# Kernel optimization log

Hardware: AMD Instinct MI355X
Metric: run time of the kernel (lower is better)

The kernel has to match this reference:

```python
import jax, jax.numpy as jnp
import numpy as np

BLOCK = 16.0  # BLOCK_X == BLOCK_Y == 16


def setup_inputs() -> dict:
    key = jax.random.key(0)
    k1, k2, k3 = jax.random.split(key, 3)
    N = 4_000_000
    means3D = jax.random.normal(k1, (N, 3), dtype=jnp.float32)
    scales = jax.random.uniform(k2, (N, 3), dtype=jnp.float32, minval=0.005, maxval=0.05)
    rotations = jax.random.normal(k3, (N, 4), dtype=jnp.float32)  # unnormalized quats (r,x,y,z)
    # row-vector convention: p' = [x,y,z,1] @ M  (matches matrix[0]*x + matrix[4]*y + ... indexing)
    tanfovx, tanfovy = 0.8, 0.45
    znear, zfar = 0.01, 100.0
    view = np.eye(4, dtype=np.float32)
    view[3, 2] = 8.0  # camera translation: all points end up in front of camera
    proj_cam = np.zeros((4, 4), dtype=np.float32)
    proj_cam[0, 0] = 1.0 / tanfovx
    proj_cam[1, 1] = 1.0 / tanfovy
    proj_cam[2, 2] = zfar / (zfar - znear)
    proj_cam[2, 3] = 1.0
    proj_cam[3, 2] = -zfar * znear / (zfar - znear)
    projmatrix = view @ proj_cam  # full (view*proj), as in 3DGS
    return {
        "means3D": means3D,
        "scales": scales,
        "rotations": rotations,
        "viewmatrix": jnp.asarray(view),
        "projmatrix": jnp.asarray(projmatrix),
        "tanfovx": tanfovx,
        "tanfovy": tanfovy,
        "scale_modifier": 1.0,
        "image_height": 1080,
        "image_width": 1920,
    }


def reference(means3D, scales, rotations, viewmatrix, projmatrix,
              tanfovx, tanfovy, scale_modifier, image_height, image_width):
    H = float(image_height)
    W = float(image_width)
    focal_x = W / (2.0 * tanfovx)
    focal_y = H / (2.0 * tanfovy)

    # ---- projection (transformPoint4x3 / 4x4, row-vector convention) ----
    p_view = means3D @ viewmatrix[:3, :3] + viewmatrix[3, :3]        # [N,3]
    p_hom = means3D @ projmatrix[:3, :] + projmatrix[3, :]           # [N,4]
    p_w = 1.0 / (p_hom[:, 3] + 1e-7)
    p_proj = p_hom[:, :3] * p_w[:, None]

    # ---- computeCov3D: Sigma = (S R)^T (S R) ----
    r, x, y, z = rotations[:, 0], rotations[:, 1], rotations[:, 2], rotations[:, 3]
    R = jnp.stack([
        jnp.stack([1.0 - 2.0 * (y * y + z * z), 2.0 * (x * y - r * z), 2.0 * (x * z + r * y)], axis=-1),
        jnp.stack([2.0 * (x * y + r * z), 1.0 - 2.0 * (x * x + z * z), 2.0 * (y * z - r * x)], axis=-1),
        jnp.stack([2.0 * (x * z - r * y), 2.0 * (y * z + r * x), 1.0 - 2.0 * (x * x + y * y)], axis=-1),
    ], axis=-2)                                                      # [N,3,3]
    M = (scale_modifier * scales)[:, :, None] * R                    # S @ R: scale rows
    Sigma = jnp.einsum('nki,nkj->nij', M, M)                         # M^T M, symmetric [N,3,3]

    # ---- computeCov2D: EWA splatting Jacobian ----
    tz = p_view[:, 2]
    limx = 1.3 * tanfovx
    limy = 1.3 * tanfovy
    tx = jnp.clip(p_view[:, 0] / tz, -limx, limx) * tz
    ty = jnp.clip(p_view[:, 1] / tz, -limy, limy) * tz
    zeros = jnp.zeros_like(tz)
    # only the first two columns of J matter for the 2x2 cov
    col0 = jnp.stack([focal_x / tz, zeros, -(focal_x * tx) / (tz * tz)], axis=-1)  # [N,3]
    col1 = jnp.stack([zeros, focal_y / tz, -(focal_y * ty) / (tz * tz)], axis=-1)
    Jc = jnp.stack([col0, col1], axis=-1)                            # [N,3,2]
    W3 = viewmatrix[:3, :3]                                          # 3x3 rotation block
    T2 = jnp.einsum('ij,njk->nik', W3, Jc)                           # [N,3,2]
    cov2 = jnp.einsum('nki,nkl,nlj->nij', T2, Sigma, T2)             # [N,2,2]
    cov_x = cov2[:, 0, 0] + 0.3
    cov_y = cov2[:, 0, 1]
    cov_z = cov2[:, 1, 1] + 0.3

    # ---- screen-space radius from eigenvalues ----
    det = cov_x * cov_z - cov_y * cov_y
    mid = 0.5 * (cov_x + cov_z)
    lambda1 = mid + jnp.sqrt(jnp.maximum(0.1, mid * mid - det))      # lambda1 >= lambda2 always
    radius = jnp.ceil(3.0 * jnp.sqrt(lambda1))

    # ---- tile rect test (getRect) ----
    px = ((p_proj[:, 0] + 1.0) * W - 1.0) * 0.5                      # ndc2Pix
    py = ((p_proj[:, 1] + 1.0) * H - 1.0) * 0.5
    gx = (W + BLOCK - 1.0) / BLOCK
    gy = (H + BLOCK - 1.0) / BLOCK
    rmin_x = jnp.clip(jnp.floor((px - radius) / BLOCK), 0.0, gx)
    rmin_y = jnp.clip(jnp.floor((py - radius) / BLOCK), 0.0, gy)
    rmax_x = jnp.clip(jnp.floor((px + radius + BLOCK - 1.0) / BLOCK), 0.0, gx)
    rmax_y = jnp.clip(jnp.floor((py + radius + BLOCK - 1.0) / BLOCK), 0.0, gy)
    area = (rmax_x - rmin_x) * (rmax_y - rmin_y)

    # ---- culling (in_frustum + degenerate checks) ----
    valid = (tz > 0.2) & (det != 0.0) & (area != 0.0)
    radii = jnp.where(valid, radius, 0.0)
    return radii
```

## Files before the change

### kernel.cpp

```cpp
#include <hip/hip_runtime.h>


typedef float v4f __attribute__((ext_vector_type(4)));

__device__ __forceinline__ float frcp(float x)  { return __builtin_amdgcn_rcpf(x); }
__device__ __forceinline__ float fsqrt_(float x){ return __builtin_amdgcn_sqrtf(x); }

__device__ __forceinline__ v4f vrcp(v4f a) {
    v4f r; r.x = frcp(a.x); r.y = frcp(a.y); r.z = frcp(a.z); r.w = frcp(a.w); return r;
}
__device__ __forceinline__ v4f vsqrt(v4f a) {
    v4f r; r.x = fsqrt_(a.x); r.y = fsqrt_(a.y); r.z = fsqrt_(a.z); r.w = fsqrt_(a.w); return r;
}
__device__ __forceinline__ v4f vmaxs(v4f a, float b) {
    v4f r; r.x = fmaxf(a.x,b); r.y = fmaxf(a.y,b); r.z = fmaxf(a.z,b); r.w = fmaxf(a.w,b); return r;
}
__device__ __forceinline__ v4f vclamp(v4f a, float lo, float hi) {
    v4f r;
    r.x = fminf(fmaxf(a.x, lo), hi);
    r.y = fminf(fmaxf(a.y, lo), hi);
    r.z = fminf(fmaxf(a.z, lo), hi);
    r.w = fminf(fmaxf(a.w, lo), hi);
    return r;
}
__device__ __forceinline__ v4f vceil(v4f a) {
    v4f r; r.x = ceilf(a.x); r.y = ceilf(a.y); r.z = ceilf(a.z); r.w = ceilf(a.w); return r;
}

struct GaussChunk {
    v4f mx, my, mz;
    v4f qr, qx, qy, qz;
    v4f s0, s1, s2;
};

__device__ __forceinline__ v4f gauss_radii(
    const GaussChunk& c,
    const float* __restrict__ vmr, const float* __restrict__ pmr,
    float focal_x, float focal_y, float limx, float limy,
    float W, float H, float TX, float TY)
{
    const v4f pvx = c.mx*vmr[0] + c.my*vmr[4] + c.mz*vmr[8]  + vmr[12];
    const v4f pvy = c.mx*vmr[1] + c.my*vmr[5] + c.mz*vmr[9]  + vmr[13];
    const v4f tz  = c.mx*vmr[2] + c.my*vmr[6] + c.mz*vmr[10] + vmr[14];

    const v4f hx = c.mx*pmr[0] + c.my*pmr[4] + c.mz*pmr[8]  + pmr[12];
    const v4f hy = c.mx*pmr[1] + c.my*pmr[5] + c.mz*pmr[9]  + pmr[13];
    const v4f hw = c.mx*pmr[3] + c.my*pmr[7] + c.mz*pmr[11] + pmr[15];
    const v4f pw  = vrcp(hw + 1e-7f);
    const v4f ppx = hx * pw;
    const v4f ppy = hy * pw;

    const v4f itz = vrcp(tz);
    const v4f cx  = vclamp(pvx * itz, -limx, limx);
    const v4f cy  = vclamp(pvy * itz, -limy, limy);
    const v4f fxz = focal_x * itz;
    const v4f fyz = focal_y * itz;

    const v4f A0 = vmr[0] - vmr[2]*cx;
    const v4f A1 = vmr[4] - vmr[6]*cx;
    const v4f A2 = vmr[8] - vmr[10]*cx;
    const v4f B0 = vmr[1] - vmr[2]*cy;
    const v4f B1 = vmr[5] - vmr[6]*cy;
    const v4f B2 = vmr[9] - vmr[10]*cy;

    const v4f xx = c.qx*c.qx, yy = c.qy*c.qy, zz = c.qz*c.qz;
    const v4f xy = c.qx*c.qy, xz = c.qx*c.qz, yz = c.qy*c.qz;
    const v4f rx = c.qr*c.qx, ry = c.qr*c.qy, rz = c.qr*c.qz;
    const v4f R00 = 1.0f - 2.0f*(yy + zz);
    const v4f R01 = 2.0f*(xy - rz);
    const v4f R02 = 2.0f*(xz + ry);
    const v4f R10 = 2.0f*(xy + rz);
    const v4f R11 = 1.0f - 2.0f*(xx + zz);
    const v4f R12 = 2.0f*(yz - rx);
    const v4f R20 = 2.0f*(xz - ry);
    const v4f R21 = 2.0f*(yz + rx);
    const v4f R22 = 1.0f - 2.0f*(xx + yy);

    const v4f e0 = c.s0 * (R00*A0 + R01*A1 + R02*A2);
    const v4f e1 = c.s1 * (R10*A0 + R11*A1 + R12*A2);
    const v4f e2 = c.s2 * (R20*A0 + R21*A1 + R22*A2);
    const v4f f0 = c.s0 * (R00*B0 + R01*B1 + R02*B2);
    const v4f f1 = c.s1 * (R10*B0 + R11*B1 + R12*B2);
    const v4f f2 = c.s2 * (R20*B0 + R21*B1 + R22*B2);
    const v4f ee = e0*e0 + e1*e1 + e2*e2;
    const v4f ef = e0*f0 + e1*f1 + e2*f2;
    const v4f ff = f0*f0 + f1*f1 + f2*f2;

    const v4f cov_x = fxz*fxz*ee + 0.3f;
    const v4f cov_y = fxz*fyz*ef;
    const v4f cov_z = fyz*fyz*ff + 0.3f;
    const v4f det = cov_x*cov_z - cov_y*cov_y;
    const v4f mid = 0.5f*(cov_x + cov_z);
    const v4f lambda1 = mid + vsqrt(vmaxs(mid*mid - det, 0.1f));
    const v4f radius = vceil(3.0f * vsqrt(lambda1));

    const v4f pxs = ((ppx + 1.0f)*W - 1.0f)*0.5f;
    const v4f pys = ((ppy + 1.0f)*H - 1.0f)*0.5f;

    v4f res;
    #pragma unroll
    for (int u = 0; u < 4; ++u) {
        const float rad = radius[u];
        const float pxu = pxs[u], pyu = pys[u];
        const bool vx = ((pxu + rad + 15.0f) >= 16.0f) && ((pxu - rad) < TX);
        const bool vy = ((pyu + rad + 15.0f) >= 16.0f) && ((pyu - rad) < TY);
        const bool valid = (tz[u] > 0.2f) && (det[u] != 0.0f) && vx && vy;
        res[u] = valid ? rad : 0.0f;
    }
    return res;
}

__global__ __launch_bounds__(256) void gauss_pre_kernel(
    const float* __restrict__ means,
    const float* __restrict__ scales,
    const float* __restrict__ rots,
    const float* __restrict__ vm,
    const float* __restrict__ pm,
    const float* __restrict__ s_tanfovx,
    const float* __restrict__ s_tanfovy,
    const float* __restrict__ s_scmod,
    const int*   __restrict__ s_ih,
    const int*   __restrict__ s_iw,
    float* __restrict__ out,
    int n)
{
    const int t  = blockIdx.x * blockDim.x + threadIdx.x;
    const int g0 = t * 8;
    if (g0 >= n) return;

    const float tanfovx = s_tanfovx[0];
    const float tanfovy = s_tanfovy[0];
    const float scmod   = s_scmod[0];
    const float H = (float)s_ih[0];
    const float W = (float)s_iw[0];
    const float focal_x = W * 0.5f * frcp(tanfovx);
    const float focal_y = H * 0.5f * frcp(tanfovy);
    const float limx = 1.3f * tanfovx;
    const float limy = 1.3f * tanfovy;
    const float gx = (W + 15.0f) * 0.0625f;
    const float gy = (H + 15.0f) * 0.0625f;
    const float TX = 16.0f * ceilf(gx);
    const float TY = 16.0f * ceilf(gy);

    float vmr[16], pmr[16];
    #pragma unroll
    for (int i = 0; i < 4; ++i) {
        float4 a = ((const float4*)vm)[i];
        vmr[4*i+0] = a.x; vmr[4*i+1] = a.y; vmr[4*i+2] = a.z; vmr[4*i+3] = a.w;
        float4 b = ((const float4*)pm)[i];
        pmr[4*i+0] = b.x; pmr[4*i+1] = b.y; pmr[4*i+2] = b.z; pmr[4*i+3] = b.w;
    }

    GaussChunk ch[2];
    const bool full = (g0 + 7 < n);
    if (full) {
        const float4* m4 = (const float4*)means  + (size_t)t * 6;
        const float4* s4 = (const float4*)scales + (size_t)t * 6;
        const float4* r4 = (const float4*)rots   + (size_t)t * 8;
        const float4 m0 = m4[0], m1 = m4[1], m2 = m4[2], m3 = m4[3], m5 = m4[4], m6 = m4[5];
        const float4 sA = s4[0], sB = s4[1], sC = s4[2], sD = s4[3], sE = s4[4], sF = s4[5];
        const float4 r0 = r4[0], r1 = r4[1], r2 = r4[2], r3 = r4[3];
        const float4 r5 = r4[4], r6 = r4[5], r7 = r4[6], r8 = r4[7];

        ch[0].mx = (v4f){m0.x, m0.w, m1.z, m2.y};
        ch[0].my = (v4f){m0.y, m1.x, m1.w, m2.z};
        ch[0].mz = (v4f){m0.z, m1.y, m2.x, m2.w};
        ch[1].mx = (v4f){m3.x, m3.w, m5.z, m6.y};
        ch[1].my = (v4f){m3.y, m5.x, m5.w, m6.z};
        ch[1].mz = (v4f){m3.z, m5.y, m6.x, m6.w};

        ch[0].s0 = scmod * (v4f){sA.x, sA.w, sB.z, sC.y};
        ch[0].s1 = scmod * (v4f){sA.y, sB.x, sB.w, sC.z};
        ch[0].s2 = scmod * (v4f){sA.z, sB.y, sC.x, sC.w};
        ch[1].s0 = scmod * (v4f){sD.x, sD.w, sE.z, sF.y};
        ch[1].s1 = scmod * (v4f){sD.y, sE.x, sE.w, sF.z};
        ch[1].s2 = scmod * (v4f){sD.z, sE.y, sF.x, sF.w};

        ch[0].qr = (v4f){r0.x, r1.x, r2.x, r3.x};
        ch[0].qx = (v4f){r0.y, r1.y, r2.y, r3.y};
        ch[0].qy = (v4f){r0.z, r1.z, r2.z, r3.z};
        ch[0].qz = (v4f){r0.w, r1.w, r2.w, r3.w};
        ch[1].qr = (v4f){r5.x, r6.x, r7.x, r8.x};
        ch[1].qx = (v4f){r5.y, r6.y, r7.y, r8.y};
        ch[1].qy = (v4f){r5.z, r6.z, r7.z, r8.z};
        ch[1].qz = (v4f){r5.w, r6.w, r7.w, r8.w};
    } else {
        #pragma unroll
        for (int h = 0; h < 2; ++h) {
            #pragma unroll
            for (int u = 0; u < 4; ++u) {
                const int g = g0 + h*4 + u;
                float mv[3] = {0.f, 0.f, 0.f};
                float sv[3] = {0.f, 0.f, 0.f};
                float qv[4] = {1.f, 0.f, 0.f, 0.f};
                if (g < n) {
                    mv[0] = means[3*(size_t)g+0];
                    mv[1] = means[3*(size_t)g+1];
                    mv[2] = means[3*(size_t)g+2];
                    sv[0] = scales[3*(size_t)g+0];
                    sv[1] = scales[3*(size_t)g+1];
                    sv[2] = scales[3*(size_t)g+2];
                    qv[0] = rots[4*(size_t)g+0];
                    qv[1] = rots[4*(size_t)g+1];
                    qv[2] = rots[4*(size_t)g+2];
                    qv[3] = rots[4*(size_t)g+3];
                }
                ch[h].mx[u] = mv[0]; ch[h].my[u] = mv[1]; ch[h].mz[u] = mv[2];
                ch[h].s0[u] = scmod*sv[0]; ch[h].s1[u] = scmod*sv[1]; ch[h].s2[u] = scmod*sv[2];
                ch[h].qr[u] = qv[0]; ch[h].qx[u] = qv[1];
                ch[h].qy[u] = qv[2]; ch[h].qz[u] = qv[3];
            }
        }
    }

    v4f res0 = gauss_radii(ch[0], vmr, pmr, focal_x, focal_y, limx, limy, W, H, TX, TY);
    v4f res1 = gauss_radii(ch[1], vmr, pmr, focal_x, focal_y, limx, limy, W, H, TX, TY);

    if (full) {
        __builtin_nontemporal_store(res0, (v4f*)out + 2*(size_t)t);
        __builtin_nontemporal_store(res1, (v4f*)out + 2*(size_t)t + 1);
    } else {
        #pragma unroll
        for (int u = 0; u < 4; ++u) {
            if (g0 + u < n) out[g0 + u] = res0[u];
        }
        #pragma unroll
        for (int u = 0; u < 4; ++u) {
            if (g0 + 4 + u < n) out[g0 + 4 + u] = res1[u];
        }
    }
}

extern "C" void kernel_launch(void* const* d_in, const int* in_sizes, int n_in,
                              void* d_out, int out_size, void* d_ws, size_t ws_size,
                              hipStream_t stream) {
    const float* means  = (const float*)d_in[0];
    const float* scales = (const float*)d_in[1];
    const float* rots   = (const float*)d_in[2];
    const float* vm     = (const float*)d_in[3];
    const float* pm     = (const float*)d_in[4];
    const float* tfx    = (const float*)d_in[5];
    const float* tfy    = (const float*)d_in[6];
    const float* scm    = (const float*)d_in[7];
    const int*   ih     = (const int*)d_in[8];
    const int*   iw     = (const int*)d_in[9];
    float* out = (float*)d_out;

    const int n  = in_sizes[0] / 3;
    const int n8 = (n + 7) / 8;
    dim3 block(256);
    dim3 grid((n8 + 255) / 256);
    hipLaunchKernelGGL(gauss_pre_kernel, grid, block, 0, stream,
                       means, scales, rots, vm, pm, tfx, tfy, scm, ih, iw, out, n);
}
```

Baseline: 31.66 us.

## Use persistent grid-stride loop with double-buffered software-prefetched loads

The kernel now launches a fixed grid of up to 1024 blocks that loops over the data in grid-stride order, four Gaussians per thread per step. The loads for the next chunk are issued before the current chunk is computed, using two register buffers, so memory latency can overlap with arithmetic. The aim is to amortise per-thread setup and hide load latency. In exchange, each thread holds more registers, and the strided access pattern across blocks may reduce coalescing locality.

```diff
diff --git a/kernel.cpp b/kernel.cpp
--- a/kernel.cpp
+++ b/kernel.cpp
@@ -27,18 +27,38 @@
     v4f r; r.x = ceilf(a.x); r.y = ceilf(a.y); r.z = ceilf(a.z); r.w = ceilf(a.w); return r;
 }
 
+struct Raw4 {
+    float4 m0, m1, m2;
+    float4 s0, s1, s2;
+    float4 r0, r1, r2, r3;
+};
+
 struct GaussChunk {
     v4f mx, my, mz;
     v4f qr, qx, qy, qz;
     v4f s0, s1, s2;
 };
 
-__device__ __forceinline__ v4f gauss_radii(
-    const GaussChunk& c,
-    const float* __restrict__ vmr, const float* __restrict__ pmr,
-    float focal_x, float focal_y, float limx, float limy,
-    float W, float H, float TX, float TY)
-{
+struct Cam {
+    float vmr[16], pmr[16];
+    float focal_x, focal_y, limx, limy, W, H, TX, TY, scmod;
+};
+
+__device__ __forceinline__ void load4(Raw4& g,
+    const float4* __restrict__ m4, const float4* __restrict__ s4,
+    const float4* __restrict__ r4, int t)
+{
+    const size_t t3 = (size_t)t * 3, t4 = (size_t)t * 4;
+    g.m0 = m4[t3];   g.m1 = m4[t3+1]; g.m2 = m4[t3+2];
+    g.s0 = s4[t3];   g.s1 = s4[t3+1]; g.s2 = s4[t3+2];
+    g.r0 = r4[t4];   g.r1 = r4[t4+1]; g.r2 = r4[t4+2]; g.r3 = r4[t4+3];
+}
+
+__device__ __forceinline__ v4f gauss_radii(const GaussChunk& c, const Cam& K)
+{
+    const float* vmr = K.vmr;
+    const float* pmr = K.pmr;
+
     const v4f pvx = c.mx*vmr[0] + c.my*vmr[4] + c.mz*vmr[8]  + vmr[12];
     const v4f pvy = c.mx*vmr[1] + c.my*vmr[5] + c.mz*vmr[9]  + vmr[13];
     const v4f tz  = c.mx*vmr[2] + c.my*vmr[6] + c.mz*vmr[10] + vmr[14];
@@ -51,10 +71,10 @@
     const v4f ppy = hy * pw;
 
     const v4f itz = vrcp(tz);
-    const v4f cx  = vclamp(pvx * itz, -limx, limx);
-    const v4f cy  = vclamp(pvy * itz, -limy, limy);
-    const v4f fxz = focal_x * itz;
-    const v4f fyz = focal_y * itz;
+    const v4f cx  = vclamp(pvx * itz, -K.limx, K.limx);
+    const v4f cy  = vclamp(pvy * itz, -K.limy, K.limy);
+    const v4f fxz = K.focal_x * itz;
+    const v4f fyz = K.focal_y * itz;
 
     const v4f A0 = vmr[0] - vmr[2]*cx;
     const v4f A1 = vmr[4] - vmr[6]*cx;
@@ -94,20 +114,64 @@
     const v4f lambda1 = mid + vsqrt(vmaxs(mid*mid - det, 0.1f));
     const v4f radius = vceil(3.0f * vsqrt(lambda1));
 
-    const v4f pxs = ((ppx + 1.0f)*W - 1.0f)*0.5f;
-    const v4f pys = ((ppy + 1.0f)*H - 1.0f)*0.5f;
+    const v4f pxs = ((ppx + 1.0f)*K.W - 1.0f)*0.5f;
+    const v4f pys = ((ppy + 1.0f)*K.H - 1.0f)*0.5f;
 
     v4f res;
     #pragma unroll
     for (int u = 0; u < 4; ++u) {
         const float rad = radius[u];
         const float pxu = pxs[u], pyu = pys[u];
-        const bool vx = ((pxu + rad + 15.0f) >= 16.0f) && ((pxu - rad) < TX);
-        const bool vy = ((pyu + rad + 15.0f) >= 16.0f) && ((pyu - rad) < TY);
+        const bool vx = ((pxu + rad + 15.0f) >= 16.0f) && ((pxu - rad) < K.TX);
+        const bool vy = ((pyu + rad + 15.0f) >= 16.0f) && ((pyu - rad) < K.TY);
         const bool valid = (tz[u] > 0.2f) && (det[u] != 0.0f) && vx && vy;
         res[u] = valid ? rad : 0.0f;
     }
     return res;
+}
+
+__device__ __forceinline__ void process4(
+    const Raw4& g, bool full, int t,
+    const float* __restrict__ means, const float* __restrict__ scales,
+    const float* __restrict__ rots, float* __restrict__ out,
+    const Cam& K, int n)
+{
+    GaussChunk c;
+    if (full) {
+        c.mx = (v4f){g.m0.x, g.m0.w, g.m1.z, g.m2.y};
+        c.my = (v4f){g.m0.y, g.m1.x, g.m1.w, g.m2.z};
+        c.mz = (v4f){g.m0.z, g.m1.y, g.m2.x, g.m2.w};
+        c.s0 = K.scmod * (v4f){g.s0.x, g.s0.w, g.s1.z, g.s2.y};
+        c.s1 = K.scmod * (v4f){g.s0.y, g.s1.x, g.s1.w, g.s2.z};
+        c.s2 = K.scmod * (v4f){g.s0.z, g.s1.y, g.s2.x, g.s2.w};
+        c.qr = (v4f){g.r0.x, g.r1.x, g.r2.x, g.r3.x};
+        c.qx = (v4f){g.r0.y, g.r1.y, g.r2.y, g.r3.y};
+        c.qy = (v4f){g.r0.z, g.r1.z, g.r2.z, g.r3.z};
+        c.qz = (v4f){g.r0.w, g.r1.w, g.r2.w, g.r3.w};
+    } else {
+        #pragma unroll
+        for (int u = 0; u < 4; ++u) {
+            const int gi = 4*t + u;
+            float mv[3] = {0.f,0.f,0.f}, sv[3] = {0.f,0.f,0.f}, qv[4] = {1.f,0.f,0.f,0.f};
+            if (gi < n) {
+                mv[0]=means[3*(size_t)gi]; mv[1]=means[3*(size_t)gi+1]; mv[2]=means[3*(size_t)gi+2];
+                sv[0]=scales[3*(size_t)gi]; sv[1]=scales[3*(size_t)gi+1]; sv[2]=scales[3*(size_t)gi+2];
+                qv[0]=rots[4*(size_t)gi]; qv[1]=rots[4*(size_t)gi+1];
+                qv[2]=rots[4*(size_t)gi+2]; qv[3]=rots[4*(size_t)gi+3];
+            }
+            c.mx[u]=mv[0]; c.my[u]=mv[1]; c.mz[u]=mv[2];
+            c.s0[u]=K.scmod*sv[0]; c.s1[u]=K.scmod*sv[1]; c.s2[u]=K.scmod*sv[2];
+            c.qr[u]=qv[0]; c.qx[u]=qv[1]; c.qy[u]=qv[2]; c.qz[u]=qv[3];
+        }
+    }
+    const v4f res = gauss_radii(c, K);
+    if (full) {
+        __builtin_nontemporal_store(res, (v4f*)out + t);
+    } else {
+        #pragma unroll
+        for (int u = 0; u < 4; ++u)
+            if (4*t + u < n) out[4*t + u] = res[u];
+    }
 }
 
 __global__ __launch_bounds__(256) void gauss_pre_kernel(
@@ -124,110 +188,56 @@
     float* __restrict__ out,
     int n)
 {
-    const int t  = blockIdx.x * blockDim.x + threadIdx.x;
-    const int g0 = t * 8;
-    if (g0 >= n) return;
-
+    const int n4 = (n + 3) >> 2;
+    int t = blockIdx.x * blockDim.x + threadIdx.x;
+    if (t >= n4) return;
+    const int T = gridDim.x * blockDim.x;
+
+    Cam K;
+    K.scmod = s_scmod[0];
     const float tanfovx = s_tanfovx[0];
     const float tanfovy = s_tanfovy[0];
-    const float scmod   = s_scmod[0];
-    const float H = (float)s_ih[0];
-    const float W = (float)s_iw[0];
-    const float focal_x = W * 0.5f * frcp(tanfovx);
-    const float focal_y = H * 0.5f * frcp(tanfovy);
-    const float limx = 1.3f * tanfovx;
-    const float limy = 1.3f * tanfovy;
-    const float gx = (W + 15.0f) * 0.0625f;
-    const float gy = (H + 15.0f) * 0.0625f;
-    const float TX = 16.0f * ceilf(gx);
-    const float TY = 16.0f * ceilf(gy);
-
-    float vmr[16], pmr[16];
+    K.H = (float)s_ih[0];
+    K.W = (float)s_iw[0];
+    K.focal_x = K.W * 0.5f * frcp(tanfovx);
+    K.focal_y = K.H * 0.5f * frcp(tanfovy);
+    K.limx = 1.3f * tanfovx;
+    K.limy = 1.3f * tanfovy;
+    K.TX = 16.0f * ceilf((K.W + 15.0f) * 0.0625f);
+    K.TY = 16.0f * ceilf((K.H + 15.0f) * 0.0625f);
     #pragma unroll
     for (int i = 0; i < 4; ++i) {
         float4 a = ((const float4*)vm)[i];
-        vmr[4*i+0] = a.x; vmr[4*i+1] = a.y; vmr[4*i+2] = a.z; vmr[4*i+3] = a.w;
+        K.vmr[4*i+0]=a.x; K.vmr[4*i+1]=a.y; K.vmr[4*i+2]=a.z; K.vmr[4*i+3]=a.w;
         float4 b = ((const float4*)pm)[i];
-        pmr[4*i+0] = b.x; pmr[4*i+1] = b.y; pmr[4*i+2] = b.z; pmr[4*i+3] = b.w;
-    }
-
-    GaussChunk ch[2];
-    const bool full = (g0 + 7 < n);
-    if (full) {
-        const float4* m4 = (const float4*)means  + (size_t)t * 6;
-        const float4* s4 = (const float4*)scales + (size_t)t * 6;
-        const float4* r4 = (const float4*)rots   + (size_t)t * 8;
-        const float4 m0 = m4[0], m1 = m4[1], m2 = m4[2], m3 = m4[3], m5 = m4[4], m6 = m4[5];
-        const float4 sA = s4[0], sB = s4[1], sC = s4[2], sD = s4[3], sE = s4[4], sF = s4[5];
-        const float4 r0 = r4[0], r1 = r4[1], r2 = r4[2], r3 = r4[3];
-        const float4 r5 = r4[4], r6 = r4[5], r7 = r4[6], r8 = r4[7];
-
-        ch[0].mx = (v4f){m0.x, m0.w, m1.z, m2.y};
-        ch[0].my = (v4f){m0.y, m1.x, m1.w, m2.z};
-        ch[0].mz = (v4f){m0.z, m1.y, m2.x, m2.w};
-        ch[1].mx = (v4f){m3.x, m3.w, m5.z, m6.y};
-        ch[1].my = (v4f){m3.y, m5.x, m5.w, m6.z};
-        ch[1].mz = (v4f){m3.z, m5.y, m6.x, m6.w};
-
-        ch[0].s0 = scmod * (v4f){sA.x, sA.w, sB.z, sC.y};
-        ch[0].s1 = scmod * (v4f){sA.y, sB.x, sB.w, sC.z};
-        ch[0].s2 = scmod * (v4f){sA.z, sB.y, sC.x, sC.w};
-        ch[1].s0 = scmod * (v4f){sD.x, sD.w, sE.z, sF.y};
-        ch[1].s1 = scmod * (v4f){sD.y, sE.x, sE.w, sF.z};
-        ch[1].s2 = scmod * (v4f){sD.z, sE.y, sF.x, sF.w};
-
-        ch[0].qr = (v4f){r0.x, r1.x, r2.x, r3.x};
-        ch[0].qx = (v4f){r0.y, r1.y, r2.y, r3.y};
-        ch[0].qy = (v4f){r0.z, r1.z, r2.z, r3.z};
-        ch[0].qz = (v4f){r0.w, r1.w, r2.w, r3.w};
-        ch[1].qr = (v4f){r5.x, r6.x, r7.x, r8.x};
-        ch[1].qx = (v4f){r5.y, r6.y, r7.y, r8.y};
-        ch[1].qy = (v4f){r5.z, r6.z, r7.z, r8.z};
-        ch[1].qz = (v4f){r5.w, r6.w, r7.w, r8.w};
-    } else {
-        #pragma unroll
-        for (int h = 0; h < 2; ++h) {
-            #pragma unroll
-            for (int u = 0; u < 4; ++u) {
-                const int g = g0 + h*4 + u;
-                float mv[3] = {0.f, 0.f, 0.f};
-                float sv[3] = {0.f, 0.f, 0.f};
-                float qv[4] = {1.f, 0.f, 0.f, 0.f};
-                if (g < n) {
-                    mv[0] = means[3*(size_t)g+0];
-                    mv[1] = means[3*(size_t)g+1];
-                    mv[2] = means[3*(size_t)g+2];
-                    sv[0] = scales[3*(size_t)g+0];
-                    sv[1] = scales[3*(size_t)g+1];
-                    sv[2] = scales[3*(size_t)g+2];
-                    qv[0] = rots[4*(size_t)g+0];
-                    qv[1] = rots[4*(size_t)g+1];
-                    qv[2] = rots[4*(size_t)g+2];
-                    qv[3] = rots[4*(size_t)g+3];
-                }
-                ch[h].mx[u] = mv[0]; ch[h].my[u] = mv[1]; ch[h].mz[u] = mv[2];
-                ch[h].s0[u] = scmod*sv[0]; ch[h].s1[u] = scmod*sv[1]; ch[h].s2[u] = scmod*sv[2];
-                ch[h].qr[u] = qv[0]; ch[h].qx[u] = qv[1];
-                ch[h].qy[u] = qv[2]; ch[h].qz[u] = qv[3];
-            }
-        }
-    }
-
-    v4f res0 = gauss_radii(ch[0], vmr, pmr, focal_x, focal_y, limx, limy, W, H, TX, TY);
-    v4f res1 = gauss_radii(ch[1], vmr, pmr, focal_x, focal_y, limx, limy, W, H, TX, TY);
-
-    if (full) {
-        __builtin_nontemporal_store(res0, (v4f*)out + 2*(size_t)t);
-        __builtin_nontemporal_store(res1, (v4f*)out + 2*(size_t)t + 1);
-    } else {
-        #pragma unroll
-        for (int u = 0; u < 4; ++u) {
-            if (g0 + u < n) out[g0 + u] = res0[u];
-        }
-        #pragma unroll
-        for (int u = 0; u < 4; ++u) {
-            if (g0 + 4 + u < n) out[g0 + 4 + u] = res1[u];
-        }
+        K.pmr[4*i+0]=b.x; K.pmr[4*i+1]=b.y; K.pmr[4*i+2]=b.z; K.pmr[4*i+3]=b.w;
+    }
+
+    const float4* m4 = (const float4*)means;
+    const float4* s4 = (const float4*)scales;
+    const float4* r4 = (const float4*)rots;
+
+    Raw4 bufA, bufB;
+    bool fullA = (4*(size_t)t + 3 < (size_t)n);
+    if (fullA) load4(bufA, m4, s4, r4, t);
+
+    for (;;) {
+        const int tB = t + T;
+        const bool hasB = tB < n4;
+        const bool fullB = hasB && (4*(size_t)tB + 3 < (size_t)n);
+        if (fullB) load4(bufB, m4, s4, r4, tB);
+        process4(bufA, fullA, t, means, scales, rots, out, K, n);
+        if (!hasB) break;
+
+        const int tA = tB + T;
+        const bool hasA = tA < n4;
+        const bool fullA2 = hasA && (4*(size_t)tA + 3 < (size_t)n);
+        if (fullA2) load4(bufA, m4, s4, r4, tA);
+        process4(bufB, fullB, tB, means, scales, rots, out, K, n);
+        if (!hasA) break;
+
+        t = tA;
+        fullA = fullA2;
     }
 }
 
@@ -246,10 +256,13 @@
     const int*   iw     = (const int*)d_in[9];
     float* out = (float*)d_out;
 
-    const int n  = in_sizes[0] / 3;
-    const int n8 = (n + 7) / 8;
+    const int n = in_sizes[0] / 3;
+    const int n4 = (n + 3) / 4;
+    int nblocks = 1024;
+    const int maxb = (n4 + 255) / 256;
+    if (nblocks > maxb) nblocks = maxb;
     dim3 block(256);
-    dim3 grid((n8 + 255) / 256);
+    dim3 grid(nblocks);
     hipLaunchKernelGGL(gauss_pre_kernel, grid, block, 0, stream,
                        means, scales, rots, vm, pm, tfx, tfy, scm, ih, iw, out, n);
 }
```

Result: slower. 63.53 us (+100.7%).
